# Optimization experiments

Measured on AMD Instinct MI355X. Metric: run time of the kernel, lower is better.

The kernel has to match this reference:

```python
import jax, jax.numpy as jnp
import numpy as np

D_MODEL = 256; D_FC = 1024; N_LEVELS = 4; N_HEADS = 8; N_POINTS = 4
D_HEAD = D_MODEL // N_HEADS
SPATIAL = np.array([[100, 100], [50, 50], [25, 25], [13, 13]], dtype=np.int64)
S_TOTAL = int((SPATIAL[:, 0] * SPATIAL[:, 1]).sum())  # 13294
BATCH = 2


def setup_inputs() -> dict:
    key = jax.random.key(0)
    ks = jax.random.split(key, 16)

    def lin(k, fi, fo):
        s = 1.0 / np.sqrt(fi)
        kw, kb = jax.random.split(k)
        W = jax.random.uniform(kw, (fi, fo), jnp.float32, -s, s)
        b = jax.random.uniform(kb, (fo,), jnp.float32, -s, s)
        return W, b

    W_off, b_off = lin(ks[0], D_MODEL, N_HEADS * N_LEVELS * N_POINTS * 2)
    W_attn, b_attn = lin(ks[1], D_MODEL, N_HEADS * N_LEVELS * N_POINTS)
    W_val, b_val = lin(ks[2], D_MODEL, D_MODEL)
    W_out, b_out = lin(ks[3], D_MODEL, D_MODEL)
    W1, b1 = lin(ks[4], D_MODEL, D_FC)
    W2, b2 = lin(ks[5], D_FC, D_MODEL)
    src = jax.random.normal(ks[6], (BATCH, S_TOTAL, D_MODEL), jnp.float32)
    pos = jax.random.normal(ks[7], (BATCH, S_TOTAL, D_MODEL), jnp.float32)
    reference_points = jax.random.uniform(ks[8], (BATCH, S_TOTAL, N_LEVELS, 2), jnp.float32)
    level_start_index = np.concatenate([[0], np.cumsum(SPATIAL[:, 0] * SPATIAL[:, 1])[:-1]]).astype(np.int64)
    return dict(src=src, pos=pos, reference_points=reference_points,
                spatial_shapes=SPATIAL, level_start_index=level_start_index,
                W_off=W_off, b_off=b_off, W_attn=W_attn, b_attn=b_attn,
                W_val=W_val, b_val=b_val, W_out=W_out, b_out=b_out,
                ln1_g=jnp.ones(D_MODEL, jnp.float32), ln1_b=jnp.zeros(D_MODEL, jnp.float32),
                W1=W1, b1=b1, W2=W2, b2=b2,
                ln2_g=jnp.ones(D_MODEL, jnp.float32), ln2_b=jnp.zeros(D_MODEL, jnp.float32))


def layernorm(x, g, b, eps=1e-5):
    mu = x.mean(-1, keepdims=True)
    var = ((x - mu) ** 2).mean(-1, keepdims=True)
    return (x - mu) * jax.lax.rsqrt(var + eps) * g + b


def ms_deform_attn(query, value_in, ref_pts, shapes,
                   W_off, b_off, W_attn, b_attn, W_val, b_val, W_out, b_out):
    N, Lq, _ = query.shape
    value = (value_in @ W_val + b_val).reshape(N, -1, N_HEADS, D_HEAD)
    off = (query @ W_off + b_off).reshape(N, Lq, N_HEADS, N_LEVELS, N_POINTS, 2)
    attn = (query @ W_attn + b_attn).reshape(N, Lq, N_HEADS, N_LEVELS * N_POINTS)
    attn = jax.nn.softmax(attn, -1).reshape(N, Lq, N_HEADS, N_LEVELS, N_POINTS)
    # offset normalizer is (W_l, H_l) per level
    norm = jnp.array([[w, h] for (h, w) in shapes], dtype=query.dtype)
    loc = ref_pts[:, :, None, :, None, :] + off / norm[None, None, None, :, None, :]
    out = jnp.zeros((N, Lq, N_HEADS, D_HEAD), query.dtype)
    start = 0
    for l, (H_, W_) in enumerate(shapes):
        v = value[:, start:start + H_ * W_].transpose(0, 2, 1, 3)  # [N, heads, HW, d]
        start += H_ * W_
        loc_l = loc[:, :, :, l]  # [N, Lq, heads, P, 2]
        # grid_sample(align_corners=False, padding_mode='zeros'): pixel = loc*size - 0.5
        px = loc_l[..., 0] * W_ - 0.5
        py = loc_l[..., 1] * H_ - 0.5
        x0 = jnp.floor(px); y0 = jnp.floor(py)
        wx = (px - x0)[..., None]; wy = (py - y0)[..., None]
        x0i = x0.astype(jnp.int32); y0i = y0.astype(jnp.int32)

        def samp(xi, yi):
            valid = (xi >= 0) & (xi < W_) & (yi >= 0) & (yi < H_)
            idx = jnp.clip(yi, 0, H_ - 1) * W_ + jnp.clip(xi, 0, W_ - 1)  # [N,Lq,heads,P]
            idx = idx.transpose(0, 2, 1, 3).reshape(N, N_HEADS, Lq * N_POINTS, 1)
            g = jnp.take_along_axis(v, idx, axis=2)  # [N,heads,Lq*P,d]
            g = g.reshape(N, N_HEADS, Lq, N_POINTS, D_HEAD).transpose(0, 2, 1, 3, 4)
            return g * valid[..., None]

        val = (samp(x0i, y0i) * (1 - wx) * (1 - wy)
               + samp(x0i + 1, y0i) * wx * (1 - wy)
               + samp(x0i, y0i + 1) * (1 - wx) * wy
               + samp(x0i + 1, y0i + 1) * wx * wy)  # [N,Lq,heads,P,d]
        out = out + (val * attn[:, :, :, l, :, None]).sum(3)
    return out.reshape(N, Lq, D_MODEL) @ W_out + b_out


def reference(src, pos, reference_points, spatial_shapes, level_start_index,
              W_off, b_off, W_attn, b_attn, W_val, b_val, W_out, b_out,
              ln1_g, ln1_b, W1, b1, W2, b2, ln2_g, ln2_b):
    shapes = [(int(spatial_shapes[l, 0]), int(spatial_shapes[l, 1])) for l in range(N_LEVELS)]
    q = src + pos
    attn_out = ms_deform_attn(q, src, reference_points, shapes,
                              W_off, b_off, W_attn, b_attn, W_val, b_val, W_out, b_out)
    x = layernorm(src + attn_out, ln1_g, ln1_b)  # dropout is identity in eval
    ffn = jax.nn.relu(x @ W1 + b1) @ W2 + b2
    return layernorm(x + ffn, ln2_g, ln2_b)
```

## Files before the change

kernel.cpp:

```cpp
#include <hip/hip_runtime.h>
#include <hip/hip_bf16.h>

#define DM 256
#define STOT 13294
#define MTOT (2 * STOT)

using bf16 = __hip_bfloat16;
typedef __attribute__((ext_vector_type(8))) short short8;
typedef __attribute__((ext_vector_type(4))) float floatx4;

#define GLDS16(g, l) __builtin_amdgcn_global_load_lds( \
    (const __attribute__((address_space(1))) void*)(g), \
    (__attribute__((address_space(3))) void*)(l), 16, 0, 0)

__device__ __forceinline__ float bu2f(unsigned u) { return __uint_as_float(u << 16); }
__device__ __forceinline__ unsigned short f2bu(float f) {
    union { bf16 h; unsigned short u; } c; c.h = __float2bfloat16(f); return c.u;
}

__global__ void detect_dtype(const unsigned* g1, int* flag) {
    if (threadIdx.x == 0 && blockIdx.x == 0)
        *flag = (g1[0] == 0x3F800000u) ? 1 : 0;
}

struct PW { const void* W[6]; const void* B[10]; };

__global__ void prep_weights(PW a, bf16* __restrict__ WT, float* __restrict__ bf,
                             const int* __restrict__ flag) {
    const long id = (long)blockIdx.x * 256 + threadIdx.x;
    const bool f32in = (*flag != 0);
    const int sz[6]  = {65536, 65536, 32768, 65536, 262144, 262144};
    const int Ns[6]  = {256, 256, 128, 256, 1024, 256};
    const int Ksh[6] = {8, 8, 8, 8, 8, 10};
    if (id < 753664) {
        long e = id; int j = 0;
        while (e >= sz[j]) { e -= sz[j]; ++j; }
        const int n = (int)(e >> Ksh[j]);
        const int k = (int)(e & ((1 << Ksh[j]) - 1));
        const size_t src = (size_t)k * Ns[j] + n;
        float v = f32in ? ((const float*)a.W[j])[src] : __bfloat162float(((const bf16*)a.W[j])[src]);
        WT[id] = __float2bfloat16(v);
    } else if (id < 753664 + 3200) {
        long e = id - 753664; int j = 0;
        const int bsz[10] = {256, 256, 128, 256, 1024, 256, 256, 256, 256, 256};
        while (e >= bsz[j]) { e -= bsz[j]; ++j; }
        float v = f32in ? ((const float*)a.B[j])[e] : __bfloat162float(((const bf16*)a.B[j])[e]);
        bf[id - 753664] = v;
    }
}

__global__ void prep_act(const void* __restrict__ src, const void* __restrict__ pos,
                         bf16* __restrict__ sbf, bf16* __restrict__ qbf,
                         const int* __restrict__ flag) {
    const long i = ((long)blockIdx.x * 256 + threadIdx.x) * 8;
    if (i >= (long)MTOT * DM) return;
    unsigned short ps[8], pq[8];
    if (*flag) {
        const float* s = (const float*)src + i;
        const float* p = (const float*)pos + i;
        float4 a0 = *(const float4*)s, a1 = *(const float4*)(s + 4);
        float4 b0 = *(const float4*)p, b1 = *(const float4*)(p + 4);
        const float av[8] = {a0.x, a0.y, a0.z, a0.w, a1.x, a1.y, a1.z, a1.w};
        const float bv[8] = {b0.x, b0.y, b0.z, b0.w, b1.x, b1.y, b1.z, b1.w};
#pragma unroll
        for (int j = 0; j < 8; ++j) { ps[j] = f2bu(av[j]); pq[j] = f2bu(av[j] + bv[j]); }
    } else {
        const unsigned short* s = (const unsigned short*)src + i;
        const unsigned short* p = (const unsigned short*)pos + i;
        uint4 a = *(const uint4*)s, b = *(const uint4*)p;
        const unsigned* ua = (const unsigned*)&a;
        const unsigned* ub = (const unsigned*)&b;
#pragma unroll
        for (int j = 0; j < 4; ++j) {
            float a0 = bu2f(ua[j] & 0xffffu), a1 = bu2f(ua[j] >> 16);
            float b0 = bu2f(ub[j] & 0xffffu), b1 = bu2f(ub[j] >> 16);
            ps[j * 2] = f2bu(a0); ps[j * 2 + 1] = f2bu(a1);
            pq[j * 2] = f2bu(a0 + b0); pq[j * 2 + 1] = f2bu(a1 + b1);
        }
    }
    *(uint4*)((unsigned short*)sbf + i) = *(const uint4*)ps;
    *(uint4*)((unsigned short*)qbf + i) = *(const uint4*)pq;
}

template<bool RELU>
__global__ __launch_bounds__(256, 4)
void gemm_bf16(const bf16* __restrict__ A0, const bf16* __restrict__ A1, int n_a0,
               const bf16* __restrict__ WT, const float* __restrict__ bias,
               bf16* __restrict__ C0, bf16* __restrict__ C1, bf16* __restrict__ C2,
               int M, int N, int K, int ldc0, int vtM) {
    __shared__ __align__(16) bf16 sh[16384];
    const int t = threadIdx.x;
    const int wave = t >> 6, lane = t & 63;
    const int bm = blockIdx.y * 128, bn = blockIdx.x * 128;
    const bf16* __restrict__ A = (bn < n_a0) ? A0 : A1;
    const int wm = (wave >> 1) * 64, wn = (wave & 1) * 64;
    const int l15 = lane & 15, quad = lane >> 4;
    const int srow = lane >> 2, sko = (lane & 3) * 8;

    floatx4 acc[4][4];
#pragma unroll
    for (int i = 0; i < 4; ++i)
#pragma unroll
        for (int j = 0; j < 4; ++j) acc[i][j] = (floatx4)0.f;

    const int nb = K >> 5;
#pragma unroll
    for (int rh = 0; rh < 2; ++rh) {
        const int rbase = rh * 64 + wave * 16;
        const int gm = min(bm + rbase + srow, M - 1);
        GLDS16(A + (size_t)gm * K + sko, &sh[rbase * 32]);
        GLDS16(WT + (size_t)(bn + rbase + srow) * K + sko, &sh[8192 + rbase * 32]);
    }
    for (int i = 0; i < nb; ++i) {
        __syncthreads();
        if (i + 1 < nb) {
            const int k0 = (i + 1) << 5;
            const int bo = ((i + 1) & 1) * 4096;
#pragma unroll
            for (int rh = 0; rh < 2; ++rh) {
                const int rbase = rh * 64 + wave * 16;
                const int gm = min(bm + rbase + srow, M - 1);
                GLDS16(A + (size_t)gm * K + k0 + sko, &sh[bo + rbase * 32]);
                GLDS16(WT + (size_t)(bn + rbase + srow) * K + k0 + sko, &sh[8192 + bo + rbase * 32]);
            }
        }
        const int bo = (i & 1) * 4096;
        short8 af[4], bfr[4];
#pragma unroll
        for (int mi = 0; mi < 4; ++mi)
            af[mi] = *(const short8*)&sh[bo + (wm + mi * 16 + l15) * 32 + quad * 8];
#pragma unroll
        for (int nj = 0; nj < 4; ++nj)
            bfr[nj] = *(const short8*)&sh[8192 + bo + (wn + nj * 16 + l15) * 32 + quad * 8];
#pragma unroll
        for (int mi = 0; mi < 4; ++mi)
#pragma unroll
            for (int nj = 0; nj < 4; ++nj)
                acc[mi][nj] = __builtin_amdgcn_mfma_f32_16x16x32_bf16(bfr[nj], af[mi], acc[mi][nj], 0, 0, 0);
    }

    bf16* C = C0; int coloff = bn, ldc = ldc0; bool vt = false;
    if (C1 != nullptr && bn >= 256) {
        if (C2 != nullptr && bn >= 512) { C = C2; coloff = bn - 512; ldc = 128; }
        else                            { C = C1; coloff = bn - 256; ldc = 256; }
    } else {
        vt = (vtM > 0);
    }
    float4 bv4[4];
#pragma unroll
    for (int nj = 0; nj < 4; ++nj)
        bv4[nj] = *(const float4*)&bias[bn + wn + nj * 16 + quad * 4];
#pragma unroll
    for (int mi = 0; mi < 4; ++mi) {
        const int gm = bm + wm + mi * 16 + l15;
        if (gm >= M) continue;
#pragma unroll
        for (int nj = 0; nj < 4; ++nj) {
            const float bb[4] = {bv4[nj].x, bv4[nj].y, bv4[nj].z, bv4[nj].w};
            unsigned short pk[4];
#pragma unroll
            for (int r = 0; r < 4; ++r) {
                float v = acc[mi][nj][r] + bb[r];
                if (RELU) v = fmaxf(v, 0.f);
                pk[r] = f2bu(v);
            }
            const int n = coloff + wn + nj * 16 + quad * 4;
            if (vt) {
                *(uint2*)&C[((size_t)(n >> 5) * vtM + gm) * 32 + (n & 31)] = *(const uint2*)pk;
            } else {
                *(uint2*)&C[(size_t)gm * ldc + n] = *(const uint2*)pk;
            }
        }
    }
}

__global__ void softmax16(bf16* __restrict__ a, int total) {
    const int i = blockIdx.x * 256 + threadIdx.x;
    if (i >= total) return;
    unsigned short* p = (unsigned short*)(a + (size_t)i * 16);
    uint4 r0 = *(const uint4*)p, r1 = *(const uint4*)(p + 8);
    float w[16];
    const unsigned* u0 = (const unsigned*)&r0;
    const unsigned* u1 = (const unsigned*)&r1;
#pragma unroll
    for (int j = 0; j < 4; ++j) {
        w[j * 2] = bu2f(u0[j] & 0xffffu); w[j * 2 + 1] = bu2f(u0[j] >> 16);
        w[8 + j * 2] = bu2f(u1[j] & 0xffffu); w[8 + j * 2 + 1] = bu2f(u1[j] >> 16);
    }
    float mx = -1e30f;
#pragma unroll
    for (int j = 0; j < 16; ++j) mx = fmaxf(mx, w[j]);
    float s = 0.f;
#pragma unroll
    for (int j = 0; j < 16; ++j) { w[j] = __expf(w[j] - mx); s += w[j]; }
    const float inv = 1.f / s;
    unsigned short pk[16];
#pragma unroll
    for (int j = 0; j < 16; ++j) pk[j] = f2bu(w[j] * inv);
    *(uint4*)p = *(const uint4*)pk;
    *(uint4*)(p + 8) = *(const uint4*)(pk + 8);
}

__global__ __launch_bounds__(256)
void deform_sample(const bf16* __restrict__ valueT, const bf16* __restrict__ off,
                   const bf16* __restrict__ attw, const void* __restrict__ refp,
                   bf16* __restrict__ out, const int* __restrict__ flag) {
    __shared__ int4   sIdx[512];
    __shared__ float4 sWt[512];
    const int t = threadIdx.x;
    const bool f32r = (*flag != 0);

#pragma unroll
    for (int r = 0; r < 2; ++r) {
        const int e = t + r * 256;
        const int ql = e >> 7, rem = e & 127;
        const int h = rem & 7, j = rem >> 3;
        const int l = j >> 2;
        const int q = blockIdx.x * 4 + ql;
        const int b = (q >= STOT) ? 1 : 0;
        const int Ws4[4] = {100, 50, 25, 13};
        const int Ls4[4] = {0, 10000, 12500, 13125};

        const unsigned op = *(const unsigned*)((const unsigned short*)off + (size_t)q * 256 + h * 32 + j * 2);
        const float ox = bu2f(op & 0xffffu), oy = bu2f(op >> 16);
        const float aw = bu2f(((const unsigned short*)attw)[(size_t)q * 128 + h * 16 + j]);
        float rx, ry;
        if (f32r) {
            const float* rp = (const float*)refp + (size_t)q * 8 + l * 2;
            rx = rp[0]; ry = rp[1];
        } else {
            const unsigned short* rp = (const unsigned short*)refp + (size_t)q * 8 + l * 2;
            rx = bu2f(rp[0]); ry = bu2f(rp[1]);
        }
        const int W_ = Ws4[l];
        const float fw = (float)W_;
        const float px = rx * fw + ox - 0.5f;
        const float py = ry * fw + oy - 0.5f;
        const float x0f = floorf(px), y0f = floorf(py);
        const float wx = px - x0f, wy = py - y0f;
        const int x0 = (int)x0f, y0 = (int)y0f;
        const float ex = 1.f - wx, ey = 1.f - wy;
        const int rowb = h * MTOT + b * STOT + Ls4[l];
        const int xs[2] = {x0, x0 + 1}, ys[2] = {y0, y0 + 1};
        const float fx[2] = {ex, wx}, fy[2] = {ey, wy};
        int idxv[4]; float wv[4];
#pragma unroll
        for (int cy = 0; cy < 2; ++cy)
#pragma unroll
            for (int cx = 0; cx < 2; ++cx) {
                const int xi = xs[cx], yi = ys[cy];
                const bool valid = (xi >= 0) & (xi < W_) & (yi >= 0) & (yi < W_);
                const int xc = min(max(xi, 0), W_ - 1);
                const int yc = min(max(yi, 0), W_ - 1);
                idxv[cy * 2 + cx] = (rowb + yc * W_ + xc) << 6;
                wv[cy * 2 + cx] = valid ? fx[cx] * fy[cy] * aw : 0.f;
            }
        const int slot = ql * 128 + rem;
        sIdx[slot] = make_int4(idxv[0], idxv[1], idxv[2], idxv[3]);
        sWt[slot] = make_float4(wv[0], wv[1], wv[2], wv[3]);
    }
    __syncthreads();

    const int ql = t >> 6, ln = t & 63;
    const int h = ln >> 3, dg = ln & 7;
    const int side = dg >> 2, cg = dg & 3;
    const int q = blockIdx.x * 4 + ql;
    const char* vbytes = (const char*)valueT;
    const unsigned lo = (unsigned)(cg * 16);
    const int sbase = ql * 128 + h;

    float acc[8];
#pragma unroll
    for (int i = 0; i < 8; ++i) acc[i] = 0.f;

#pragma unroll 2
    for (int jc = 0; jc < 4; ++jc) {
        uint4 vd[8]; float wgt[8];
#pragma unroll
        for (int u = 0; u < 4; ++u) {
            const int j = jc * 4 + u;
            const int4 iv = sIdx[sbase + j * 8];
            const float4 wv = sWt[sbase + j * 8];
            const int ia = side ? iv.y : iv.x;
            const int ib = side ? iv.w : iv.z;
            vd[u * 2]     = *(const uint4*)(vbytes + (unsigned)ia + lo);
            vd[u * 2 + 1] = *(const uint4*)(vbytes + (unsigned)ib + lo);
            wgt[u * 2]     = side ? wv.y : wv.x;
            wgt[u * 2 + 1] = side ? wv.w : wv.z;
        }
#pragma unroll
        for (int u = 0; u < 8; ++u) {
            const unsigned* pv = (const unsigned*)&vd[u];
            const float wq = wgt[u];
#pragma unroll
            for (int c = 0; c < 4; ++c) {
                acc[c * 2]     = fmaf(wq, __uint_as_float(pv[c] << 16), acc[c * 2]);
                acc[c * 2 + 1] = fmaf(wq, __uint_as_float(pv[c] & 0xffff0000u), acc[c * 2 + 1]);
            }
        }
    }
#pragma unroll
    for (int i = 0; i < 8; ++i) acc[i] += __shfl_xor(acc[i], 4, 64);
    unsigned short pk[4];
#pragma unroll
    for (int r = 0; r < 4; ++r) pk[r] = f2bu(acc[side * 4 + r]);
    *(uint2*)((unsigned short*)out + (size_t)q * 256 + h * 32 + cg * 8 + side * 4) = *(const uint2*)pk;
}

__global__ __launch_bounds__(512, 1)
void out_ln1(const bf16* __restrict__ vsamp, const bf16* __restrict__ srcbf,
             const bf16* __restrict__ WoT, const float* __restrict__ bo_f,
             const float* __restrict__ g1, const float* __restrict__ be1,
             bf16* __restrict__ vx, int M) {
    __shared__ __align__(16) bf16 Bs[8 * 4096];
    const int t = threadIdx.x, wave = t >> 6, lane = t & 63;
    const int l15 = lane & 15, quad = lane >> 4;
    const int srow = lane >> 2, sko = (lane & 3) * 8;
    const int bm = blockIdx.x * 128;
    const int mrow = bm + wave * 16 + l15;
    const int mc = min(mrow, M - 1);

    short8 af[8];
#pragma unroll
    for (int kk = 0; kk < 8; ++kk)
        af[kk] = *(const short8*)(vsamp + (size_t)mc * 256 + kk * 32 + quad * 8);

    floatx4 acc[16];
#pragma unroll
    for (int i = 0; i < 16; ++i) acc[i] = (floatx4)0.f;

    for (int nc = 0; nc < 2; ++nc) {
        __syncthreads();
#pragma unroll
        for (int rr = 0; rr < 8; ++rr)
            GLDS16(WoT + (size_t)(nc * 128 + rr * 16 + srow) * 256 + wave * 32 + sko,
                   &Bs[wave * 4096 + rr * 512]);
        __syncthreads();
#pragma unroll
        for (int kk = 0; kk < 8; ++kk)
#pragma unroll
            for (int nj = 0; nj < 8; ++nj) {
                short8 bfr = *(const short8*)&Bs[kk * 4096 + (nj * 16 + l15) * 32 + quad * 8];
                acc[nc * 8 + nj] = __builtin_amdgcn_mfma_f32_16x16x32_bf16(bfr, af[kk], acc[nc * 8 + nj], 0, 0, 0);
            }
    }

    float s = 0.f;
#pragma unroll
    for (int nj = 0; nj < 16; ++nj) {
        const int n = nj * 16 + quad * 4;
        const float4 bo = *(const float4*)&bo_f[n];
        const uint2 ru = *(const uint2*)(srcbf + (size_t)mc * 256 + n);
        const float rs[4] = {bu2f(ru.x & 0xffffu), bu2f(ru.x >> 16), bu2f(ru.y & 0xffffu), bu2f(ru.y >> 16)};
        const float bb[4] = {bo.x, bo.y, bo.z, bo.w};
#pragma unroll
        for (int r = 0; r < 4; ++r) { acc[nj][r] += bb[r] + rs[r]; s += acc[nj][r]; }
    }
    s += __shfl_xor(s, 16, 64); s += __shfl_xor(s, 32, 64);
    const float mean = s * (1.f / 256.f);
    float s2 = 0.f;
#pragma unroll
    for (int nj = 0; nj < 16; ++nj)
#pragma unroll
        for (int r = 0; r < 4; ++r) { const float c = acc[nj][r] - mean; s2 += c * c; }
    s2 += __shfl_xor(s2, 16, 64); s2 += __shfl_xor(s2, 32, 64);
    const float rstd = rsqrtf(s2 * (1.f / 256.f) + 1e-5f);
    if (mrow < M) {
#pragma unroll
        for (int nj = 0; nj < 16; ++nj) {
            const int n = nj * 16 + quad * 4;
            const float4 g = *(const float4*)&g1[n];
            const float4 b = *(const float4*)&be1[n];
            const float gg[4] = {g.x, g.y, g.z, g.w}, bb[4] = {b.x, b.y, b.z, b.w};
            unsigned short pk[4];
#pragma unroll
            for (int r = 0; r < 4; ++r) pk[r] = f2bu((acc[nj][r] - mean) * rstd * gg[r] + bb[r]);
            *(uint2*)&vx[(size_t)mrow * 256 + n] = *(const uint2*)pk;
        }
    }
}

__global__ __launch_bounds__(256, 2)
void ffn_ln2(const bf16* __restrict__ vx, const bf16* __restrict__ W1T, const bf16* __restrict__ W2T,
             const float* __restrict__ b1f, const float* __restrict__ b2f,
             const float* __restrict__ g2, const float* __restrict__ be2,
             void* __restrict__ outp, const int* __restrict__ flag, int M) {
    __shared__ __align__(16) bf16 Bs1[16384];
    __shared__ __align__(16) bf16 Bs2[8192];
    __shared__ __align__(16) bf16 Hs[64 * 136];
    __shared__ float2 red[128];
    const int t = threadIdx.x, wv = t >> 6, lane = t & 63;
    const int l15 = lane & 15, quad = lane >> 4;
    const int g = wv & 1, nh = wv >> 1;
    const int srow = lane >> 2, sko = (lane & 3) * 8;
    const int bm = blockIdx.x * 64;

    int mrow[2], mc[2];
#pragma unroll
    for (int mi = 0; mi < 2; ++mi) {
        mrow[mi] = bm + g * 32 + mi * 16 + l15;
        mc[mi] = min(mrow[mi], M - 1);
    }
    short8 af[2][8];
#pragma unroll
    for (int mi = 0; mi < 2; ++mi)
#pragma unroll
        for (int kk = 0; kk < 8; ++kk)
            af[mi][kk] = *(const short8*)(vx + (size_t)mc[mi] * 256 + kk * 32 + quad * 8);

    floatx4 acc2[2][8];
#pragma unroll
    for (int mi = 0; mi < 2; ++mi)
#pragma unroll
        for (int nj = 0; nj < 8; ++nj) acc2[mi][nj] = (floatx4)0.f;

    for (int ch = 0; ch < 8; ++ch) {
        floatx4 acc1[2][4];
#pragma unroll
        for (int mi = 0; mi < 2; ++mi)
#pragma unroll
            for (int nj = 0; nj < 4; ++nj) acc1[mi][nj] = (floatx4)0.f;
#pragma unroll
        for (int ks = 0; ks < 2; ++ks) {
            __syncthreads();
#pragma unroll
            for (int j = 0; j < 8; ++j)
                GLDS16(W1T + (size_t)(ch * 128 + j * 16 + srow) * 256 + ks * 128 + wv * 32 + sko,
                       &Bs1[wv * 4096 + j * 512]);
            __syncthreads();
#pragma unroll
            for (int kk = 0; kk < 4; ++kk) {
                short8 bfr[4];
#pragma unroll
                for (int nj = 0; nj < 4; ++nj)
                    bfr[nj] = *(const short8*)&Bs1[kk * 4096 + (nh * 64 + nj * 16 + l15) * 32 + quad * 8];
#pragma unroll
                for (int mi = 0; mi < 2; ++mi)
#pragma unroll
                    for (int nj = 0; nj < 4; ++nj)
                        acc1[mi][nj] = __builtin_amdgcn_mfma_f32_16x16x32_bf16(bfr[nj], af[mi][ks * 4 + kk], acc1[mi][nj], 0, 0, 0);
            }
        }
#pragma unroll
        for (int mi = 0; mi < 2; ++mi)
#pragma unroll
            for (int nj = 0; nj < 4; ++nj) {
                const int kl = nh * 64 + nj * 16 + quad * 4;
                const float4 bb = *(const float4*)&b1f[ch * 128 + kl];
                const float bv[4] = {bb.x, bb.y, bb.z, bb.w};
                unsigned short pk[4];
#pragma unroll
                for (int r = 0; r < 4; ++r) pk[r] = f2bu(fmaxf(acc1[mi][nj][r] + bv[r], 0.f));
                *(uint2*)&Hs[(g * 32 + mi * 16 + l15) * 136 + kl] = *(const uint2*)pk;
            }
#pragma unroll
        for (int p = 0; p < 4; ++p) {
            __syncthreads();
#pragma unroll
            for (int j = 0; j < 4; ++j)
                GLDS16(W2T + (size_t)(wv * 64 + j * 16 + srow) * 1024 + ch * 128 + p * 32 + sko,
                       &Bs2[(wv * 64 + j * 16) * 32]);
            __syncthreads();
            short8 ah[2];
#pragma unroll
            for (int mi = 0; mi < 2; ++mi)
                ah[mi] = *(const short8*)&Hs[(g * 32 + mi * 16 + l15) * 136 + p * 32 + quad * 8];
#pragma unroll
            for (int nj = 0; nj < 8; ++nj) {
                short8 bfr = *(const short8*)&Bs2[(nh * 128 + nj * 16 + l15) * 32 + quad * 8];
#pragma unroll
                for (int mi = 0; mi < 2; ++mi)
                    acc2[mi][nj] = __builtin_amdgcn_mfma_f32_16x16x32_bf16(bfr, ah[mi], acc2[mi][nj], 0, 0, 0);
            }
        }
    }

    float sm[2] = {0.f, 0.f}, sq[2] = {0.f, 0.f};
#pragma unroll
    for (int mi = 0; mi < 2; ++mi)
#pragma unroll
        for (int nj = 0; nj < 8; ++nj) {
            const int n = nh * 128 + nj * 16 + quad * 4;
            const float4 bo = *(const float4*)&b2f[n];
            const uint2 ru = *(const uint2*)(vx + (size_t)mc[mi] * 256 + n);
            const float rs[4] = {bu2f(ru.x & 0xffffu), bu2f(ru.x >> 16), bu2f(ru.y & 0xffffu), bu2f(ru.y >> 16)};
            const float bb[4] = {bo.x, bo.y, bo.z, bo.w};
#pragma unroll
            for (int r = 0; r < 4; ++r) {
                const float v = acc2[mi][nj][r] + bb[r] + rs[r];
                acc2[mi][nj][r] = v; sm[mi] += v; sq[mi] += v * v;
            }
        }
#pragma unroll
    for (int mi = 0; mi < 2; ++mi) {
        sm[mi] += __shfl_xor(sm[mi], 16, 64); sm[mi] += __shfl_xor(sm[mi], 32, 64);
        sq[mi] += __shfl_xor(sq[mi], 16, 64); sq[mi] += __shfl_xor(sq[mi], 32, 64);
    }
    __syncthreads();
    if (quad == 0) {
#pragma unroll
        for (int mi = 0; mi < 2; ++mi)
            red[((nh * 2 + g) * 2 + mi) * 16 + l15] = make_float2(sm[mi], sq[mi]);
    }
    __syncthreads();
    const bool f32o = (*flag != 0);
#pragma unroll
    for (int mi = 0; mi < 2; ++mi) {
        const float2 o = red[(((1 - nh) * 2 + g) * 2 + mi) * 16 + l15];
        const float ts = sm[mi] + o.x, tq = sq[mi] + o.y;
        const float mean = ts * (1.f / 256.f);
        const float var = tq * (1.f / 256.f) - mean * mean;
        const float rstd = rsqrtf(var + 1e-5f);
        if (mrow[mi] < M) {
#pragma unroll
            for (int nj = 0; nj < 8; ++nj) {
                const int n = nh * 128 + nj * 16 + quad * 4;
                const float4 gv = *(const float4*)&g2[n];
                const float4 bv = *(const float4*)&be2[n];
                const float gg[4] = {gv.x, gv.y, gv.z, gv.w}, bb[4] = {bv.x, bv.y, bv.z, bv.w};
                float y[4];
#pragma unroll
                for (int r = 0; r < 4; ++r) y[r] = (acc2[mi][nj][r] - mean) * rstd * gg[r] + bb[r];
                if (f32o) {
                    float4 ov = {y[0], y[1], y[2], y[3]};
                    *(float4*)((float*)outp + (size_t)mrow[mi] * 256 + n) = ov;
                } else {
                    unsigned short pk[4] = {f2bu(y[0]), f2bu(y[1]), f2bu(y[2]), f2bu(y[3])};
                    *(uint2*)((bf16*)outp + (size_t)mrow[mi] * 256 + n) = *(const uint2*)pk;
                }
            }
        }
    }
}

extern "C" void kernel_launch(void* const* d_in, const int* in_sizes, int n_in,
                              void* d_out, int out_size, void* d_ws, size_t ws_size,
                              hipStream_t stream) {
    const void* src   = d_in[0];
    const void* pos   = d_in[1];
    const void* refp  = d_in[2];
    const void* W_off = d_in[5];
    const void* b_off = d_in[6];
    const void* W_att = d_in[7];
    const void* b_att = d_in[8];
    const void* W_val = d_in[9];
    const void* b_val = d_in[10];
    const void* W_out = d_in[11];
    const void* b_out = d_in[12];
    const void* ln1g  = d_in[13];
    const void* ln1b  = d_in[14];
    const void* W1    = d_in[15];
    const void* b1    = d_in[16];
    const void* W2    = d_in[17];
    const void* b2    = d_in[18];
    const void* ln2g  = d_in[19];
    const void* ln2b  = d_in[20];

    const size_t M = MTOT;
    bf16* src_bf = (bf16*)d_ws;
    bf16* q_bf   = src_bf + M * 256;
    bf16* v_val  = src_bf + M * 512;
    bf16* v_off  = src_bf + M * 768;
    bf16* v_attn = src_bf + M * 1024;
    bf16* v_samp = src_bf + M * 1152;
    bf16* v_x    = src_bf + M * 1408;
    bf16* WT     = src_bf + M * 1664;
    float* biasf = (float*)(WT + 753664);
    int* flag    = (int*)(biasf + 3200);

    dim3 blk(256);
    const int mg = (MTOT + 127) / 128;

    detect_dtype<<<1, 64, 0, stream>>>((const unsigned*)ln1g, flag);

    PW pw;
    pw.W[0] = W_val; pw.W[1] = W_off; pw.W[2] = W_att; pw.W[3] = W_out; pw.W[4] = W1; pw.W[5] = W2;
    pw.B[0] = b_val; pw.B[1] = b_off; pw.B[2] = b_att; pw.B[3] = b_out; pw.B[4] = b1; pw.B[5] = b2;
    pw.B[6] = ln1g;  pw.B[7] = ln1b;  pw.B[8] = ln2g;  pw.B[9] = ln2b;
    prep_weights<<<(753664 + 3200 + 255) / 256, blk, 0, stream>>>(pw, WT, biasf, flag);
    prep_act<<<(int)((M * 256 / 8 + 255) / 256), blk, 0, stream>>>(src, pos, src_bf, q_bf, flag);

    gemm_bf16<false><<<dim3(5, mg), blk, 0, stream>>>(src_bf, q_bf, 256, WT, biasf,
                                                      v_val, v_off, v_attn, MTOT, 640, 256, 256, MTOT);
    softmax16<<<(MTOT * 8 + 255) / 256, blk, 0, stream>>>(v_attn, MTOT * 8);
    deform_sample<<<MTOT / 4, blk, 0, stream>>>(v_val, v_off, v_attn, refp, v_samp, flag);
    out_ln1<<<mg, dim3(512), 0, stream>>>(v_samp, src_bf, WT + 163840, biasf + 640,
                                          biasf + 2176, biasf + 2432, v_x, MTOT);
    ffn_ln2<<<(MTOT + 63) / 64, blk, 0, stream>>>(v_x, WT + 229376, WT + 491520,
                                                  biasf + 896, biasf + 1920,
                                                  biasf + 2688, biasf + 2944,
                                                  d_out, flag, MTOT);
}
```

Before: 313.6 us.

## Double-buffer FFN weight tiles and widen ffn_ln2 blocks to 128 rows

Reworks the fused FFN+LayerNorm2 kernel to use 512-thread blocks covering 128 rows, with double-buffered LDS tiles for W1 and W2. The load of the next weight tile is issued before computing on the current one. The aim is to overlap weight staging with MFMA work, halve the number of barriers per chunk, and reuse each staged weight tile across twice as many rows. In exchange, LDS use per block rises sharply and the grid shrinks to about 208 blocks, which may leave some CUs idle and lower occupancy.

Measured after the change: 310.7 us. About the same (-0.9%).

```diff
diff --git a/kernel.cpp b/kernel.cpp
--- a/kernel.cpp
+++ b/kernel.cpp
@@ -380,20 +380,21 @@
     }
 }
 
-__global__ __launch_bounds__(256, 2)
+__global__ __launch_bounds__(512, 1)
 void ffn_ln2(const bf16* __restrict__ vx, const bf16* __restrict__ W1T, const bf16* __restrict__ W2T,
              const float* __restrict__ b1f, const float* __restrict__ b2f,
              const float* __restrict__ g2, const float* __restrict__ be2,
              void* __restrict__ outp, const int* __restrict__ flag, int M) {
-    __shared__ __align__(16) bf16 Bs1[16384];
-    __shared__ __align__(16) bf16 Bs2[8192];
-    __shared__ __align__(16) bf16 Hs[64 * 136];
-    __shared__ float2 red[128];
+    __shared__ __align__(16) bf16 Bs1[2][16384];
+    __shared__ __align__(16) bf16 Bs2[2][8192];
+    __shared__ __align__(16) bf16 Hs[128 * 136];
+    __shared__ float2 red[256];
     const int t = threadIdx.x, wv = t >> 6, lane = t & 63;
     const int l15 = lane & 15, quad = lane >> 4;
-    const int g = wv & 1, nh = wv >> 1;
+    const int g = wv & 3, nh = wv >> 2;
     const int srow = lane >> 2, sko = (lane & 3) * 8;
-    const int bm = blockIdx.x * 64;
+    const int bm = blockIdx.x * 128;
+    const int kb = wv >> 1, half = wv & 1;
 
     int mrow[2], mc[2];
 #pragma unroll
@@ -414,32 +415,56 @@
 #pragma unroll
         for (int nj = 0; nj < 8; ++nj) acc2[mi][nj] = (floatx4)0.f;
 
+    auto stage1 = [&](int ch, int ks, int buf) {
+#pragma unroll
+        for (int j = 0; j < 4; ++j)
+            GLDS16(W1T + (size_t)(ch * 128 + half * 64 + j * 16 + srow) * 256 + ks * 128 + kb * 32 + sko,
+                   &Bs1[buf][kb * 4096 + (half * 64 + j * 16) * 32]);
+    };
+    auto stage2 = [&](int ch, int p, int buf) {
+#pragma unroll
+        for (int jj = 0; jj < 2; ++jj)
+            GLDS16(W2T + (size_t)(wv * 32 + jj * 16 + srow) * 1024 + ch * 128 + p * 32 + sko,
+                   &Bs2[buf][(wv * 32 + jj * 16) * 32]);
+    };
+
+    stage1(0, 0, 0);
+
     for (int ch = 0; ch < 8; ++ch) {
         floatx4 acc1[2][4];
 #pragma unroll
         for (int mi = 0; mi < 2; ++mi)
 #pragma unroll
             for (int nj = 0; nj < 4; ++nj) acc1[mi][nj] = (floatx4)0.f;
-#pragma unroll
-        for (int ks = 0; ks < 2; ++ks) {
-            __syncthreads();
-#pragma unroll
-            for (int j = 0; j < 8; ++j)
-                GLDS16(W1T + (size_t)(ch * 128 + j * 16 + srow) * 256 + ks * 128 + wv * 32 + sko,
-                       &Bs1[wv * 4096 + j * 512]);
-            __syncthreads();
-#pragma unroll
-            for (int kk = 0; kk < 4; ++kk) {
-                short8 bfr[4];
+
+        __syncthreads();
+        stage1(ch, 1, 1);
+#pragma unroll
+        for (int kk = 0; kk < 4; ++kk) {
+            short8 bfr[4];
+#pragma unroll
+            for (int nj = 0; nj < 4; ++nj)
+                bfr[nj] = *(const short8*)&Bs1[0][kk * 4096 + (nh * 64 + nj * 16 + l15) * 32 + quad * 8];
+#pragma unroll
+            for (int mi = 0; mi < 2; ++mi)
 #pragma unroll
                 for (int nj = 0; nj < 4; ++nj)
-                    bfr[nj] = *(const short8*)&Bs1[kk * 4096 + (nh * 64 + nj * 16 + l15) * 32 + quad * 8];
-#pragma unroll
-                for (int mi = 0; mi < 2; ++mi)
-#pragma unroll
-                    for (int nj = 0; nj < 4; ++nj)
-                        acc1[mi][nj] = __builtin_amdgcn_mfma_f32_16x16x32_bf16(bfr[nj], af[mi][ks * 4 + kk], acc1[mi][nj], 0, 0, 0);
-            }
+                    acc1[mi][nj] = __builtin_amdgcn_mfma_f32_16x16x32_bf16(bfr[nj], af[mi][kk], acc1[mi][nj], 0, 0, 0);
+        }
+
+        __syncthreads();
+        stage2(ch, 0, 0);
+#pragma unroll
+        for (int kk = 0; kk < 4; ++kk) {
+            short8 bfr[4];
+#pragma unroll
+            for (int nj = 0; nj < 4; ++nj)
+                bfr[nj] = *(const short8*)&Bs1[1][kk * 4096 + (nh * 64 + nj * 16 + l15) * 32 + quad * 8];
+#pragma unroll
+            for (int mi = 0; mi < 2; ++mi)
+#pragma unroll
+                for (int nj = 0; nj < 4; ++nj)
+                    acc1[mi][nj] = __builtin_amdgcn_mfma_f32_16x16x32_bf16(bfr[nj], af[mi][4 + kk], acc1[mi][nj], 0, 0, 0);
         }
 #pragma unroll
         for (int mi = 0; mi < 2; ++mi)
@@ -453,21 +478,19 @@
                 for (int r = 0; r < 4; ++r) pk[r] = f2bu(fmaxf(acc1[mi][nj][r] + bv[r], 0.f));
                 *(uint2*)&Hs[(g * 32 + mi * 16 + l15) * 136 + kl] = *(const uint2*)pk;
             }
+
 #pragma unroll
         for (int p = 0; p < 4; ++p) {
             __syncthreads();
-#pragma unroll
-            for (int j = 0; j < 4; ++j)
-                GLDS16(W2T + (size_t)(wv * 64 + j * 16 + srow) * 1024 + ch * 128 + p * 32 + sko,
-                       &Bs2[(wv * 64 + j * 16) * 32]);
-            __syncthreads();
+            if (p < 3) stage2(ch, p + 1, (p + 1) & 1);
+            else if (ch < 7) stage1(ch + 1, 0, 0);
             short8 ah[2];
 #pragma unroll
             for (int mi = 0; mi < 2; ++mi)
                 ah[mi] = *(const short8*)&Hs[(g * 32 + mi * 16 + l15) * 136 + p * 32 + quad * 8];
 #pragma unroll
             for (int nj = 0; nj < 8; ++nj) {
-                short8 bfr = *(const short8*)&Bs2[(nh * 128 + nj * 16 + l15) * 32 + quad * 8];
+                short8 bfr = *(const short8*)&Bs2[p & 1][(nh * 128 + nj * 16 + l15) * 32 + quad * 8];
 #pragma unroll
                 for (int mi = 0; mi < 2; ++mi)
                     acc2[mi][nj] = __builtin_amdgcn_mfma_f32_16x16x32_bf16(bfr, ah[mi], acc2[mi][nj], 0, 0, 0);
@@ -500,13 +523,13 @@
     if (quad == 0) {
 #pragma unroll
         for (int mi = 0; mi < 2; ++mi)
-            red[((nh * 2 + g) * 2 + mi) * 16 + l15] = make_float2(sm[mi], sq[mi]);
+            red[((nh * 4 + g) * 2 + mi) * 16 + l15] = make_float2(sm[mi], sq[mi]);
     }
     __syncthreads();
     const bool f32o = (*flag != 0);
 #pragma unroll
     for (int mi = 0; mi < 2; ++mi) {
-        const float2 o = red[(((1 - nh) * 2 + g) * 2 + mi) * 16 + l15];
+        const float2 o = red[(((1 - nh) * 4 + g) * 2 + mi) * 16 + l15];
         const float ts = sm[mi] + o.x, tq = sq[mi] + o.y;
         const float mean = ts * (1.f / 256.f);
         const float var = tq * (1.f / 256.f) - mean * mean;
@@ -586,8 +609,8 @@
     deform_sample<<<MTOT / 4, blk, 0, stream>>>(v_val, v_off, v_attn, refp, v_samp, flag);
     out_ln1<<<mg, dim3(512), 0, stream>>>(v_samp, src_bf, WT + 163840, biasf + 640,
                                           biasf + 2176, biasf + 2432, v_x, MTOT);
-    ffn_ln2<<<(MTOT + 63) / 64, blk, 0, stream>>>(v_x, WT + 229376, WT + 491520,
-                                                  biasf + 896, biasf + 1920,
-                                                  biasf + 2688, biasf + 2944,
-                                                  d_out, flag, MTOT);
-}
+    ffn_ln2<<<(MTOT + 127) / 128, dim3(512), 0, stream>>>(v_x, WT + 229376, WT + 491520,
+                                                          biasf + 896, biasf + 1920,
+                                                          biasf + 2688, biasf + 2944,
+                                                          d_out, flag, MTOT);
+}
```

## Double-buffer FFN weight tiles and XOR-swizzle LDS layouts to cut bank conflicts

Applied to the files above, without the earlier changes.

In ffn_ln2, the W1 and W2 tile staging is restructured into double-buffered LDS tiles with finer K-steps. The next tile's async global-to-LDS load is issued right after a single barrier, so it overlaps with the MFMA work on the current tile and the second barrier per step goes away. Both out_ln1 and ffn_ln2 also apply an XOR swizzle on the 16-byte column chunk, on both the staging write and the fragment read, to reduce LDS bank conflicts. The cost is extra LDS for the second buffers and reliance on the async loads having completed by the next barrier.

Result: no change. 310.0 us (-1.1%).

```diff
diff --git a/kernel.cpp b/kernel.cpp
--- a/kernel.cpp
+++ b/kernel.cpp
@@ -316,6 +316,8 @@
     const int t = threadIdx.x, wave = t >> 6, lane = t & 63;
     const int l15 = lane & 15, quad = lane >> 4;
     const int srow = lane >> 2, sko = (lane & 3) * 8;
+    const int skoS = (((lane & 3) ^ ((srow >> 1) & 3)) * 8);
+    const int qS8  = ((quad ^ ((l15 >> 1) & 3)) * 8);
     const int bm = blockIdx.x * 128;
     const int mrow = bm + wave * 16 + l15;
     const int mc = min(mrow, M - 1);
@@ -333,14 +335,14 @@
         __syncthreads();
 #pragma unroll
         for (int rr = 0; rr < 8; ++rr)
-            GLDS16(WoT + (size_t)(nc * 128 + rr * 16 + srow) * 256 + wave * 32 + sko,
+            GLDS16(WoT + (size_t)(nc * 128 + rr * 16 + srow) * 256 + wave * 32 + skoS,
                    &Bs[wave * 4096 + rr * 512]);
         __syncthreads();
 #pragma unroll
         for (int kk = 0; kk < 8; ++kk)
 #pragma unroll
             for (int nj = 0; nj < 8; ++nj) {
-                short8 bfr = *(const short8*)&Bs[kk * 4096 + (nj * 16 + l15) * 32 + quad * 8];
+                short8 bfr = *(const short8*)&Bs[kk * 4096 + (nj * 16 + l15) * 32 + qS8];
                 acc[nc * 8 + nj] = __builtin_amdgcn_mfma_f32_16x16x32_bf16(bfr, af[kk], acc[nc * 8 + nj], 0, 0, 0);
             }
     }
@@ -385,15 +387,17 @@
              const float* __restrict__ b1f, const float* __restrict__ b2f,
              const float* __restrict__ g2, const float* __restrict__ be2,
              void* __restrict__ outp, const int* __restrict__ flag, int M) {
-    __shared__ __align__(16) bf16 Bs1[16384];
-    __shared__ __align__(16) bf16 Bs2[8192];
+    __shared__ __align__(16) bf16 Bs1[2][4096];
+    __shared__ __align__(16) bf16 Bs2[2][8192];
     __shared__ __align__(16) bf16 Hs[64 * 136];
     __shared__ float2 red[128];
     const int t = threadIdx.x, wv = t >> 6, lane = t & 63;
     const int l15 = lane & 15, quad = lane >> 4;
     const int g = wv & 1, nh = wv >> 1;
-    const int srow = lane >> 2, sko = (lane & 3) * 8;
+    const int skoS = (((lane & 3) ^ ((lane >> 3) & 3)) * 8);
+    const int qS8  = ((quad ^ ((l15 >> 1) & 3)) * 8);
     const int bm = blockIdx.x * 64;
+    const int trow = t >> 2;
 
     int mrow[2], mc[2];
 #pragma unroll
@@ -414,32 +418,42 @@
 #pragma unroll
         for (int nj = 0; nj < 8; ++nj) acc2[mi][nj] = (floatx4)0.f;
 
+    auto stage1 = [&](int ch, int ks, int buf) {
+#pragma unroll
+        for (int j = 0; j < 2; ++j)
+            GLDS16(W1T + (size_t)(ch * 128 + j * 64 + trow) * 256 + ks * 32 + skoS,
+                   &Bs1[buf][(j * 64 + wv * 16) * 32]);
+    };
+    auto stage2 = [&](int ch, int p, int buf) {
+#pragma unroll
+        for (int j = 0; j < 4; ++j)
+            GLDS16(W2T + (size_t)(j * 64 + trow) * 1024 + ch * 128 + p * 32 + skoS,
+                   &Bs2[buf][(j * 64 + wv * 16) * 32]);
+    };
+
+    stage1(0, 0, 0);
+
     for (int ch = 0; ch < 8; ++ch) {
         floatx4 acc1[2][4];
 #pragma unroll
         for (int mi = 0; mi < 2; ++mi)
 #pragma unroll
             for (int nj = 0; nj < 4; ++nj) acc1[mi][nj] = (floatx4)0.f;
-#pragma unroll
-        for (int ks = 0; ks < 2; ++ks) {
+
+#pragma unroll
+        for (int ks = 0; ks < 8; ++ks) {
             __syncthreads();
-#pragma unroll
-            for (int j = 0; j < 8; ++j)
-                GLDS16(W1T + (size_t)(ch * 128 + j * 16 + srow) * 256 + ks * 128 + wv * 32 + sko,
-                       &Bs1[wv * 4096 + j * 512]);
-            __syncthreads();
-#pragma unroll
-            for (int kk = 0; kk < 4; ++kk) {
-                short8 bfr[4];
+            if (ks < 7) stage1(ch, ks + 1, (ks + 1) & 1);
+            else        stage2(ch, 0, 0);
+            short8 bfr[4];
+#pragma unroll
+            for (int nj = 0; nj < 4; ++nj)
+                bfr[nj] = *(const short8*)&Bs1[ks & 1][(nh * 64 + nj * 16 + l15) * 32 + qS8];
+#pragma unroll
+            for (int mi = 0; mi < 2; ++mi)
 #pragma unroll
                 for (int nj = 0; nj < 4; ++nj)
-                    bfr[nj] = *(const short8*)&Bs1[kk * 4096 + (nh * 64 + nj * 16 + l15) * 32 + quad * 8];
-#pragma unroll
-                for (int mi = 0; mi < 2; ++mi)
-#pragma unroll
-                    for (int nj = 0; nj < 4; ++nj)
-                        acc1[mi][nj] = __builtin_amdgcn_mfma_f32_16x16x32_bf16(bfr[nj], af[mi][ks * 4 + kk], acc1[mi][nj], 0, 0, 0);
-            }
+                    acc1[mi][nj] = __builtin_amdgcn_mfma_f32_16x16x32_bf16(bfr[nj], af[mi][ks], acc1[mi][nj], 0, 0, 0);
         }
 #pragma unroll
         for (int mi = 0; mi < 2; ++mi)
@@ -453,21 +467,19 @@
                 for (int r = 0; r < 4; ++r) pk[r] = f2bu(fmaxf(acc1[mi][nj][r] + bv[r], 0.f));
                 *(uint2*)&Hs[(g * 32 + mi * 16 + l15) * 136 + kl] = *(const uint2*)pk;
             }
+
 #pragma unroll
         for (int p = 0; p < 4; ++p) {
             __syncthreads();
-#pragma unroll
-            for (int j = 0; j < 4; ++j)
-                GLDS16(W2T + (size_t)(wv * 64 + j * 16 + srow) * 1024 + ch * 128 + p * 32 + sko,
-                       &Bs2[(wv * 64 + j * 16) * 32]);
-            __syncthreads();
+            if (p < 3)      stage2(ch, p + 1, (p + 1) & 1);
+            else if (ch < 7) stage1(ch + 1, 0, 0);
             short8 ah[2];
 #pragma unroll
             for (int mi = 0; mi < 2; ++mi)
                 ah[mi] = *(const short8*)&Hs[(g * 32 + mi * 16 + l15) * 136 + p * 32 + quad * 8];
 #pragma unroll
             for (int nj = 0; nj < 8; ++nj) {
-                short8 bfr = *(const short8*)&Bs2[(nh * 128 + nj * 16 + l15) * 32 + quad * 8];
+                short8 bfr = *(const short8*)&Bs2[p & 1][(nh * 128 + nj * 16 + l15) * 32 + qS8];
 #pragma unroll
                 for (int mi = 0; mi < 2; ++mi)
                     acc2[mi][nj] = __builtin_amdgcn_mfma_f32_16x16x32_bf16(bfr, ah[mi], acc2[mi][nj], 0, 0, 0);
```
